# Optimization experiments

Measured on AMD Instinct MI355X. Metric: run time of the kernel, lower is better.

Reference implementation:

```python
import jax, jax.numpy as jnp
import numpy as np

EMBEDDING_DIM = 10
CONTEXT_SIZE_1 = 1
CONTEXT_SIZE_2 = 3
VOCAB = 50000
N = 1_000_000
NUM_NUMERIC = 16


def setup_inputs() -> dict:
    key = jax.random.key(0)
    ks = jax.random.split(key, 9)
    text_1 = jax.random.randint(ks[0], (N,), 0, VOCAB)
    text_2 = jax.random.randint(ks[1], (N,), 0, VOCAB)
    numeric_features = jax.random.normal(ks[2], (N, NUM_NUMERIC), dtype=jnp.float32)
    emb_table_1 = jax.random.normal(ks[3], (VOCAB, EMBEDDING_DIM), dtype=jnp.float32)
    emb_table_2 = jax.random.normal(ks[4], (VOCAB, EMBEDDING_DIM), dtype=jnp.float32)
    d_in = 2 * EMBEDDING_DIM + NUM_NUMERIC
    W1 = jax.random.normal(ks[5], (d_in, 128), dtype=jnp.float32) / np.sqrt(d_in)
    b1 = jnp.zeros((128,), dtype=jnp.float32)
    W2 = jax.random.normal(ks[6], (128, 1), dtype=jnp.float32) / np.sqrt(128.0)
    b2 = jnp.zeros((1,), dtype=jnp.float32)
    return {
        "text_1": text_1,
        "text_2": text_2,
        "numeric_features": numeric_features,
        "emb_table_1": emb_table_1,
        "emb_table_2": emb_table_2,
        "W1": W1,
        "b1": b1,
        "W2": W2,
        "b2": b2,
    }


def _contextual_embedding(ids, table, context_size):
    # mean of embeddings over window [i-cs, i+cs], clipped at sequence edges
    n = ids.shape[0]
    emb = table[ids]  # [N, D] gather
    # prefix sums with leading zero row: S[j] = sum(emb[0:j])
    S = jnp.concatenate([jnp.zeros((1, emb.shape[1]), emb.dtype),
                         jnp.cumsum(emb, axis=0)], axis=0)
    pos = jnp.arange(n)
    lo = jnp.maximum(pos - context_size, 0)
    hi = jnp.minimum(pos + context_size + 1, n)
    wsum = S[hi] - S[lo]                       # [N, D]
    count = (hi - lo).astype(emb.dtype)[:, None]
    return wsum / count


def reference(text_1, text_2, numeric_features, emb_table_1, emb_table_2, W1, b1, W2, b2):
    embed_1 = _contextual_embedding(text_1, emb_table_1, CONTEXT_SIZE_1)  # [N, 10]
    embed_2 = _contextual_embedding(text_2, emb_table_2, CONTEXT_SIZE_2)  # [N, 10]
    combined = jnp.concatenate([embed_1, embed_2, numeric_features], axis=1)
    h = jax.nn.relu(combined @ W1 + b1)
    out = h @ W2 + b2
    return jax.nn.sigmoid(out)  # [N, 1]
```

## Files before the change

kernel.cpp:

```cpp
#include <hip/hip_runtime.h>
#include <hip/hip_bf16.h>

#define EMB 10
#define DIN 36
#define HID 128
#define BM  128
#define GRID 1024

typedef __attribute__((ext_vector_type(8))) short short8;
typedef __attribute__((ext_vector_type(4))) float f32x4;

union U8 { unsigned u[4]; short8 v; };

__device__ __forceinline__ short bf16_hi(float v) {
  __hip_bfloat16 h = __float2bfloat16(v);
  return *reinterpret_cast<short*>(&h);
}
__device__ __forceinline__ float bf16_to_f(short s) {
  __hip_bfloat16 h = *reinterpret_cast<__hip_bfloat16*>(&s);
  return __bfloat162float(h);
}

__device__ __forceinline__ void split_pair(float a, float b, unsigned &hi, unsigned &lo) {
  unsigned ua = __float_as_uint(a), ub = __float_as_uint(b);
  hi = __builtin_amdgcn_perm(ub, ua, 0x07060302u);
  float ra = a - __uint_as_float(ua & 0xFFFF0000u);
  float rb = b - __uint_as_float(ub & 0xFFFF0000u);
  lo = __builtin_amdgcn_perm(__float_as_uint(rb), __float_as_uint(ra), 0x07060302u);
}

__global__ void prep_kernel(const float* __restrict__ W1, const float* __restrict__ b1,
                            short* __restrict__ Bpack) {
  int b = blockIdx.x;
  int term = b >> 4;
  int ct   = (b >> 1) & 7;
  int ks   = b & 1;
  int l = threadIdx.x;
  int col = ct * 16 + (l & 15);
  int kb  = ks * 32 + (l >> 4) * 8;
  short8 o;
#pragma unroll
  for (int e = 0; e < 8; ++e) {
    int k = kb + e;
    float v = 0.0f;
    if (k < DIN)       v = W1[k * HID + col];
    else if (k == DIN) v = b1[col];
    short hb = bf16_hi(v);
    o[e] = (term == 0) ? hb : bf16_hi(v - bf16_to_f(hb));
  }
  *(short8*)(Bpack + (size_t)(((term * 8 + ct) * 2 + ks) * 64 + l) * 8) = o;
}

__global__ __launch_bounds__(256)
void fused_kernel(const int* __restrict__ t1, const int* __restrict__ t2,
                  const float* __restrict__ numf,
                  const float* __restrict__ tab1, const float* __restrict__ tab2,
                  const short* __restrict__ Bpack,
                  const float* __restrict__ W2, const float* __restrict__ b2,
                  float* __restrict__ out, int N, int ntiles) {
  __shared__ float E1[134][11];
  __shared__ float E2[136][11];
  __shared__ float Cs[BM][22];
  __shared__ short Bs[16384];

  const int tid = threadIdx.x;
  const int wid = tid >> 6, l = tid & 63;
  const int arow = l & 15, kg = l >> 4;
  const int h2 = tid - 122;

  {
    const float4* src = (const float4*)Bpack;
    float4* dst = (float4*)Bs;
#pragma unroll
    for (int i = 0; i < 8; ++i) dst[tid + 256 * i] = src[tid + 256 * i];
  }
  float w2r[8];
#pragma unroll
  for (int ct = 0; ct < 8; ++ct) w2r[ct] = W2[ct * 16 + (l & 15)];
  const float b2v = b2[0];

  const int q = ntiles / GRID, r = ntiles % GRID;
  int tbeg, tend;
  if ((int)blockIdx.x < r) { tbeg = blockIdx.x * (q + 1); tend = tbeg + q + 1; }
  else { tbeg = r * (q + 1) + ((int)blockIdx.x - r) * q; tend = tbeg + q; }

  for (int t = tbeg; t < tend; ++t) {
    const long base = (long)t * BM;

    const long rg0 = base + (long)(wid * 2) * 16 + arow;
    const long rg1 = rg0 + 16;
    float4 qa0 = {0,0,0,0}, qa1 = {0,0,0,0}, qb0 = {0,0,0,0}, qb1 = {0,0,0,0};
    if (kg == 0) {
      if (rg0 < (long)N) qa0 = *(const float4*)(numf + rg0 * 16 + 12);
      if (rg1 < (long)N) qa1 = *(const float4*)(numf + rg1 * 16 + 12);
    } else if (kg == 2) {
      if (rg0 < (long)N) qa0 = *(const float4*)(numf + rg0 * 16);
      if (rg1 < (long)N) qa1 = *(const float4*)(numf + rg1 * 16);
    } else if (kg == 3) {
      if (rg0 < (long)N) { qa0 = *(const float4*)(numf + rg0 * 16 + 4);
                           qb0 = *(const float4*)(numf + rg0 * 16 + 8); }
      if (rg1 < (long)N) { qa1 = *(const float4*)(numf + rg1 * 16 + 4);
                           qb1 = *(const float4*)(numf + rg1 * 16 + 8); }
    }

    if (tid < 130) {
      long g = base - 1 + tid;
      if (g >= 0 && g < (long)N) {
        const float2* src = (const float2*)(tab1 + (long)t1[g] * EMB);
#pragma unroll
        for (int i = 0; i < 5; ++i) {
          float2 v = src[i];
          E1[tid][2 * i] = v.x; E1[tid][2 * i + 1] = v.y;
        }
      } else {
#pragma unroll
        for (int i = 0; i < EMB; ++i) E1[tid][i] = 0.0f;
      }
    }
    if (h2 >= 0) {
      long g = base - 3 + h2;
      if (g >= 0 && g < (long)N) {
        const float2* src = (const float2*)(tab2 + (long)t2[g] * EMB);
#pragma unroll
        for (int i = 0; i < 5; ++i) {
          float2 v = src[i];
          E2[h2][2 * i] = v.x; E2[h2][2 * i + 1] = v.y;
        }
      } else {
#pragma unroll
        for (int i = 0; i < EMB; ++i) E2[h2][i] = 0.0f;
      }
    }
    __syncthreads();

    const bool edgeblk = (base == 0) || (base + BM + 3 > (long)N);
    if (tid < 120) {
      int grp = tid / 10, d = tid - grp * 10;
      int r0 = grp * 11;
      float e[13];
#pragma unroll
      for (int i = 0; i < 13; ++i) e[i] = E1[r0 + i][d];
      if (!edgeblk) {
#pragma unroll
        for (int i = 0; i < 11; ++i) {
          int rr = r0 + i;
          if (rr < BM) Cs[rr][d] = (e[i] + e[i + 1] + e[i + 2]) * (1.0f / 3.0f);
        }
      } else {
#pragma unroll
        for (int i = 0; i < 11; ++i) {
          int rr = r0 + i;
          if (rr < BM) {
            long row = base + rr;
            long lo = row - 1; if (lo < 0) lo = 0;
            long hi = row + 2; if (hi > (long)N) hi = (long)N;
            long c = hi - lo;  if (c < 1) c = 1;
            Cs[rr][d] = (e[i] + e[i + 1] + e[i + 2]) / (float)c;
          }
        }
      }
    } else if (tid < 250) {
      int u = tid - 120;
      int grp = u / 10, d = u - grp * 10;
      int r0 = grp * 10;
      float e[16];
#pragma unroll
      for (int i = 0; i < 16; ++i) e[i] = E2[r0 + i][d];
      float w = e[0] + e[1] + e[2] + e[3] + e[4] + e[5] + e[6];
      if (!edgeblk) {
#pragma unroll
        for (int i = 0; i < 10; ++i) {
          int rr = r0 + i;
          if (rr < BM) Cs[rr][10 + d] = w * (1.0f / 7.0f);
          if (i < 9) w += e[i + 7] - e[i];
        }
      } else {
#pragma unroll
        for (int i = 0; i < 10; ++i) {
          int rr = r0 + i;
          if (rr < BM) {
            long row = base + rr;
            long lo = row - 3; if (lo < 0) lo = 0;
            long hi = row + 4; if (hi > (long)N) hi = (long)N;
            long c = hi - lo;  if (c < 1) c = 1;
            Cs[rr][10 + d] = w / (float)c;
          }
          if (i < 9) w += e[i + 7] - e[i];
        }
      }
    }
    __syncthreads();

    short8 aHi[2][2], aLo[2][2];
#pragma unroll
    for (int rtl = 0; rtl < 2; ++rtl) {
      const int rr = (wid * 2 + rtl) * 16 + arow;
      const float* crow = &Cs[rr][0];
      const float4 qa = rtl ? qa1 : qa0;
      const float4 qb = rtl ? qb1 : qb0;
      U8 h0, l0, h1, l1;
      if (kg <= 1) {
#pragma unroll
        for (int i = 0; i < 4; ++i) {
          float2 tt = *(const float2*)(crow + kg * 8 + 2 * i);
          split_pair(tt.x, tt.y, h0.u[i], l0.u[i]);
        }
      } else if (kg == 2) {
        float2 t0 = *(const float2*)(crow + 16);
        float2 t1v = *(const float2*)(crow + 18);
        split_pair(t0.x, t0.y, h0.u[0], l0.u[0]);
        split_pair(t1v.x, t1v.y, h0.u[1], l0.u[1]);
        split_pair(qa.x, qa.y, h0.u[2], l0.u[2]);
        split_pair(qa.z, qa.w, h0.u[3], l0.u[3]);
      } else {
        split_pair(qa.x, qa.y, h0.u[0], l0.u[0]);
        split_pair(qa.z, qa.w, h0.u[1], l0.u[1]);
        split_pair(qb.x, qb.y, h0.u[2], l0.u[2]);
        split_pair(qb.z, qb.w, h0.u[3], l0.u[3]);
      }
      if (kg == 0) {
        split_pair(qa.x, qa.y, h1.u[0], l1.u[0]);
        split_pair(qa.z, qa.w, h1.u[1], l1.u[1]);
        h1.u[2] = 0x00003F80u; l1.u[2] = 0u;
        h1.u[3] = 0u;          l1.u[3] = 0u;
      } else {
        h1.u[0] = h1.u[1] = h1.u[2] = h1.u[3] = 0u;
        l1.u[0] = l1.u[1] = l1.u[2] = l1.u[3] = 0u;
      }
      aHi[rtl][0] = h0.v; aLo[rtl][0] = l0.v;
      aHi[rtl][1] = h1.v; aLo[rtl][1] = l1.v;
    }

    float part[2][4] = {{0,0,0,0},{0,0,0,0}};
#pragma unroll
    for (int ct = 0; ct < 8; ++ct) {
      short8 bh0 = *(const short8*)&Bs[(size_t)(((0*8 + ct)*2 + 0)*64 + l) * 8];
      short8 bh1 = *(const short8*)&Bs[(size_t)(((0*8 + ct)*2 + 1)*64 + l) * 8];
      short8 bl0 = *(const short8*)&Bs[(size_t)(((1*8 + ct)*2 + 0)*64 + l) * 8];
      short8 bl1 = *(const short8*)&Bs[(size_t)(((1*8 + ct)*2 + 1)*64 + l) * 8];
      float w2c = w2r[ct];
#pragma unroll
      for (int rtl = 0; rtl < 2; ++rtl) {
        f32x4 acc = {0.0f, 0.0f, 0.0f, 0.0f};
        acc = __builtin_amdgcn_mfma_f32_16x16x32_bf16(aHi[rtl][0], bh0, acc, 0, 0, 0);
        acc = __builtin_amdgcn_mfma_f32_16x16x32_bf16(aLo[rtl][0], bh0, acc, 0, 0, 0);
        acc = __builtin_amdgcn_mfma_f32_16x16x32_bf16(aHi[rtl][0], bl0, acc, 0, 0, 0);
        acc = __builtin_amdgcn_mfma_f32_16x16x32_bf16(aHi[rtl][1], bh1, acc, 0, 0, 0);
        acc = __builtin_amdgcn_mfma_f32_16x16x32_bf16(aLo[rtl][1], bh1, acc, 0, 0, 0);
        acc = __builtin_amdgcn_mfma_f32_16x16x32_bf16(aHi[rtl][1], bl1, acc, 0, 0, 0);
#pragma unroll
        for (int rg = 0; rg < 4; ++rg) {
          float hv = fmaxf(acc[rg], 0.0f);
          part[rtl][rg] += hv * w2c;
        }
      }
    }
#pragma unroll
    for (int off = 1; off < 16; off <<= 1) {
#pragma unroll
      for (int rtl = 0; rtl < 2; ++rtl)
#pragma unroll
        for (int rg = 0; rg < 4; ++rg)
          part[rtl][rg] += __shfl_xor(part[rtl][rg], off, 64);
    }
    if ((l & 15) < 4) {
#pragma unroll
      for (int rtl = 0; rtl < 2; ++rtl) {
        int rt = wid * 2 + rtl;
        long grow = base + rt * 16 + (l >> 4) * 4 + (l & 15);
        if (grow < (long)N) {
          float x = part[rtl][l & 15] + b2v;
          out[grow] = 1.0f / (1.0f + exp2f(x * -1.44269504f));
        }
      }
    }
  }
}

extern "C" void kernel_launch(void* const* d_in, const int* in_sizes, int n_in,
                              void* d_out, int out_size, void* d_ws, size_t ws_size,
                              hipStream_t stream) {
  const int*   t1   = (const int*)d_in[0];
  const int*   t2   = (const int*)d_in[1];
  const float* numf = (const float*)d_in[2];
  const float* tab1 = (const float*)d_in[3];
  const float* tab2 = (const float*)d_in[4];
  const float* W1   = (const float*)d_in[5];
  const float* b1   = (const float*)d_in[6];
  const float* W2   = (const float*)d_in[7];
  const float* b2   = (const float*)d_in[8];
  float* out = (float*)d_out;
  const int N = in_sizes[0];
  short* Bpack = (short*)d_ws;

  hipLaunchKernelGGL(prep_kernel, dim3(32), dim3(64), 0, stream, W1, b1, Bpack);
  int ntiles = (N + BM - 1) / BM;
  hipLaunchKernelGGL(fused_kernel, dim3(GRID), dim3(256), 0, stream,
                     t1, t2, numf, tab1, tab2, Bpack, W2, b2, out, N, ntiles);
}
```

Baseline: 208.8 us.

## Pad embedding tables to 64B rows and launch one block per tile

Adds a repack kernel that copies both embedding tables into 16-float padded rows in workspace, so each gather reads aligned float4 vectors instead of five float2 loads. The persistent grid-stride loop over tiles is replaced by one block per 128-row tile. The shared-memory copy of the packed W1 is dropped and the B fragments are read straight from global memory. The repack adds a full pass over both tables on every call, and the padded path only runs if the workspace is large enough.

Measured after the change: 247.3 us. +18.4%, slower.

```diff
diff --git a/kernel.cpp b/kernel.cpp
--- a/kernel.cpp
+++ b/kernel.cpp
@@ -5,7 +5,7 @@
 #define DIN 36
 #define HID 128
 #define BM  128
-#define GRID 1024
+#define VOCAB_MAX 50000
 
 typedef __attribute__((ext_vector_type(8))) short short8;
 typedef __attribute__((ext_vector_type(4))) float f32x4;
@@ -51,227 +51,249 @@
   *(short8*)(Bpack + (size_t)(((term * 8 + ct) * 2 + ks) * 64 + l) * 8) = o;
 }
 
+__global__ void repack_kernel(const float* __restrict__ tab1, const float* __restrict__ tab2,
+                              float* __restrict__ tp1, float* __restrict__ tp2, int vocab) {
+  int r = blockIdx.x * 256 + threadIdx.x;
+  if (r >= vocab) return;
+  const float2* s1 = (const float2*)(tab1 + (long)r * EMB);
+  const float2* s2 = (const float2*)(tab2 + (long)r * EMB);
+  float* d1 = tp1 + (long)r * 16;
+  float* d2 = tp2 + (long)r * 16;
+#pragma unroll
+  for (int i = 0; i < 5; ++i) { *(float2*)(d1 + 2 * i) = s1[i]; }
+#pragma unroll
+  for (int i = 0; i < 5; ++i) { *(float2*)(d2 + 2 * i) = s2[i]; }
+}
+
 __global__ __launch_bounds__(256)
 void fused_kernel(const int* __restrict__ t1, const int* __restrict__ t2,
                   const float* __restrict__ numf,
                   const float* __restrict__ tab1, const float* __restrict__ tab2,
+                  const float* __restrict__ tp1, const float* __restrict__ tp2,
+                  int use_padded,
                   const short* __restrict__ Bpack,
                   const float* __restrict__ W2, const float* __restrict__ b2,
-                  float* __restrict__ out, int N, int ntiles) {
-  __shared__ float E1[134][11];
-  __shared__ float E2[136][11];
+                  float* __restrict__ out, int N) {
+  __shared__ float E1[134][12];
+  __shared__ float E2[136][12];
   __shared__ float Cs[BM][22];
-  __shared__ short Bs[16384];
 
   const int tid = threadIdx.x;
+  const long base = (long)blockIdx.x * BM;
   const int wid = tid >> 6, l = tid & 63;
   const int arow = l & 15, kg = l >> 4;
-  const int h2 = tid - 122;
-
-  {
-    const float4* src = (const float4*)Bpack;
-    float4* dst = (float4*)Bs;
-#pragma unroll
-    for (int i = 0; i < 8; ++i) dst[tid + 256 * i] = src[tid + 256 * i];
+
+  const long rg0 = base + (long)(wid * 2) * 16 + arow;
+  const long rg1 = rg0 + 16;
+  float4 qa0 = {0,0,0,0}, qa1 = {0,0,0,0}, qb0 = {0,0,0,0}, qb1 = {0,0,0,0};
+  if (kg == 0) {
+    if (rg0 < (long)N) qa0 = *(const float4*)(numf + rg0 * 16 + 12);
+    if (rg1 < (long)N) qa1 = *(const float4*)(numf + rg1 * 16 + 12);
+  } else if (kg == 2) {
+    if (rg0 < (long)N) qa0 = *(const float4*)(numf + rg0 * 16);
+    if (rg1 < (long)N) qa1 = *(const float4*)(numf + rg1 * 16);
+  } else if (kg == 3) {
+    if (rg0 < (long)N) { qa0 = *(const float4*)(numf + rg0 * 16 + 4);
+                         qb0 = *(const float4*)(numf + rg0 * 16 + 8); }
+    if (rg1 < (long)N) { qa1 = *(const float4*)(numf + rg1 * 16 + 4);
+                         qb1 = *(const float4*)(numf + rg1 * 16 + 8); }
   }
   float w2r[8];
 #pragma unroll
   for (int ct = 0; ct < 8; ++ct) w2r[ct] = W2[ct * 16 + (l & 15)];
   const float b2v = b2[0];
 
-  const int q = ntiles / GRID, r = ntiles % GRID;
-  int tbeg, tend;
-  if ((int)blockIdx.x < r) { tbeg = blockIdx.x * (q + 1); tend = tbeg + q + 1; }
-  else { tbeg = r * (q + 1) + ((int)blockIdx.x - r) * q; tend = tbeg + q; }
-
-  for (int t = tbeg; t < tend; ++t) {
-    const long base = (long)t * BM;
-
-    const long rg0 = base + (long)(wid * 2) * 16 + arow;
-    const long rg1 = rg0 + 16;
-    float4 qa0 = {0,0,0,0}, qa1 = {0,0,0,0}, qb0 = {0,0,0,0}, qb1 = {0,0,0,0};
-    if (kg == 0) {
-      if (rg0 < (long)N) qa0 = *(const float4*)(numf + rg0 * 16 + 12);
-      if (rg1 < (long)N) qa1 = *(const float4*)(numf + rg1 * 16 + 12);
-    } else if (kg == 2) {
-      if (rg0 < (long)N) qa0 = *(const float4*)(numf + rg0 * 16);
-      if (rg1 < (long)N) qa1 = *(const float4*)(numf + rg1 * 16);
-    } else if (kg == 3) {
-      if (rg0 < (long)N) { qa0 = *(const float4*)(numf + rg0 * 16 + 4);
-                           qb0 = *(const float4*)(numf + rg0 * 16 + 8); }
-      if (rg1 < (long)N) { qa1 = *(const float4*)(numf + rg1 * 16 + 4);
-                           qb1 = *(const float4*)(numf + rg1 * 16 + 8); }
-    }
-
-    if (tid < 130) {
-      long g = base - 1 + tid;
-      if (g >= 0 && g < (long)N) {
-        const float2* src = (const float2*)(tab1 + (long)t1[g] * EMB);
+  if (tid < 130) {
+    long g = base - 1 + tid;
+    if (g >= 0 && g < (long)N) {
+      long idx = t1[g];
+      if (use_padded) {
+        const float4* src = (const float4*)(tp1 + idx * 16);
+        float4 q0 = src[0], q1 = src[1];
+        float2 q2 = ((const float2*)src)[4];
+        *(float4*)&E1[tid][0] = q0;
+        *(float4*)&E1[tid][4] = q1;
+        *(float2*)&E1[tid][8] = q2;
+      } else {
+        const float2* src = (const float2*)(tab1 + idx * EMB);
 #pragma unroll
         for (int i = 0; i < 5; ++i) {
           float2 v = src[i];
           E1[tid][2 * i] = v.x; E1[tid][2 * i + 1] = v.y;
         }
-      } else {
-#pragma unroll
-        for (int i = 0; i < EMB; ++i) E1[tid][i] = 0.0f;
-      }
-    }
+      }
+    } else {
+#pragma unroll
+      for (int i = 0; i < EMB; ++i) E1[tid][i] = 0.0f;
+    }
+  }
+  {
+    int h2 = tid - 122;
     if (h2 >= 0) {
       long g = base - 3 + h2;
       if (g >= 0 && g < (long)N) {
-        const float2* src = (const float2*)(tab2 + (long)t2[g] * EMB);
-#pragma unroll
-        for (int i = 0; i < 5; ++i) {
-          float2 v = src[i];
-          E2[h2][2 * i] = v.x; E2[h2][2 * i + 1] = v.y;
+        long idx = t2[g];
+        if (use_padded) {
+          const float4* src = (const float4*)(tp2 + idx * 16);
+          float4 q0 = src[0], q1 = src[1];
+          float2 q2 = ((const float2*)src)[4];
+          *(float4*)&E2[h2][0] = q0;
+          *(float4*)&E2[h2][4] = q1;
+          *(float2*)&E2[h2][8] = q2;
+        } else {
+          const float2* src = (const float2*)(tab2 + idx * EMB);
+#pragma unroll
+          for (int i = 0; i < 5; ++i) {
+            float2 v = src[i];
+            E2[h2][2 * i] = v.x; E2[h2][2 * i + 1] = v.y;
+          }
         }
       } else {
 #pragma unroll
         for (int i = 0; i < EMB; ++i) E2[h2][i] = 0.0f;
       }
     }
-    __syncthreads();
-
-    const bool edgeblk = (base == 0) || (base + BM + 3 > (long)N);
-    if (tid < 120) {
-      int grp = tid / 10, d = tid - grp * 10;
-      int r0 = grp * 11;
-      float e[13];
-#pragma unroll
-      for (int i = 0; i < 13; ++i) e[i] = E1[r0 + i][d];
-      if (!edgeblk) {
-#pragma unroll
-        for (int i = 0; i < 11; ++i) {
-          int rr = r0 + i;
-          if (rr < BM) Cs[rr][d] = (e[i] + e[i + 1] + e[i + 2]) * (1.0f / 3.0f);
+  }
+  __syncthreads();
+
+  const bool edgeblk = (base == 0) || (base + BM + 3 > (long)N);
+  if (tid < 120) {
+    int grp = tid / 10, d = tid - grp * 10;
+    int r0 = grp * 11;
+    float e[13];
+#pragma unroll
+    for (int i = 0; i < 13; ++i) e[i] = E1[r0 + i][d];
+    if (!edgeblk) {
+#pragma unroll
+      for (int i = 0; i < 11; ++i) {
+        int rr = r0 + i;
+        if (rr < BM) Cs[rr][d] = (e[i] + e[i + 1] + e[i + 2]) * (1.0f / 3.0f);
+      }
+    } else {
+#pragma unroll
+      for (int i = 0; i < 11; ++i) {
+        int rr = r0 + i;
+        if (rr < BM) {
+          long row = base + rr;
+          long lo = row - 1; if (lo < 0) lo = 0;
+          long hi = row + 2; if (hi > (long)N) hi = (long)N;
+          long c = hi - lo;  if (c < 1) c = 1;
+          Cs[rr][d] = (e[i] + e[i + 1] + e[i + 2]) / (float)c;
         }
-      } else {
-#pragma unroll
-        for (int i = 0; i < 11; ++i) {
-          int rr = r0 + i;
-          if (rr < BM) {
-            long row = base + rr;
-            long lo = row - 1; if (lo < 0) lo = 0;
-            long hi = row + 2; if (hi > (long)N) hi = (long)N;
-            long c = hi - lo;  if (c < 1) c = 1;
-            Cs[rr][d] = (e[i] + e[i + 1] + e[i + 2]) / (float)c;
-          }
+      }
+    }
+  } else if (tid < 250) {
+    int u = tid - 120;
+    int grp = u / 10, d = u - grp * 10;
+    int r0 = grp * 10;
+    float e[16];
+#pragma unroll
+    for (int i = 0; i < 16; ++i) e[i] = E2[r0 + i][d];
+    float w = e[0] + e[1] + e[2] + e[3] + e[4] + e[5] + e[6];
+    if (!edgeblk) {
+#pragma unroll
+      for (int i = 0; i < 10; ++i) {
+        int rr = r0 + i;
+        if (rr < BM) Cs[rr][10 + d] = w * (1.0f / 7.0f);
+        if (i < 9) w += e[i + 7] - e[i];
+      }
+    } else {
+#pragma unroll
+      for (int i = 0; i < 10; ++i) {
+        int rr = r0 + i;
+        if (rr < BM) {
+          long row = base + rr;
+          long lo = row - 3; if (lo < 0) lo = 0;
+          long hi = row + 4; if (hi > (long)N) hi = (long)N;
+          long c = hi - lo;  if (c < 1) c = 1;
+          Cs[rr][10 + d] = w / (float)c;
         }
-      }
-    } else if (tid < 250) {
-      int u = tid - 120;
-      int grp = u / 10, d = u - grp * 10;
-      int r0 = grp * 10;
-      float e[16];
-#pragma unroll
-      for (int i = 0; i < 16; ++i) e[i] = E2[r0 + i][d];
-      float w = e[0] + e[1] + e[2] + e[3] + e[4] + e[5] + e[6];
-      if (!edgeblk) {
-#pragma unroll
-        for (int i = 0; i < 10; ++i) {
-          int rr = r0 + i;
-          if (rr < BM) Cs[rr][10 + d] = w * (1.0f / 7.0f);
-          if (i < 9) w += e[i + 7] - e[i];
-        }
-      } else {
-#pragma unroll
-        for (int i = 0; i < 10; ++i) {
-          int rr = r0 + i;
-          if (rr < BM) {
-            long row = base + rr;
-            long lo = row - 3; if (lo < 0) lo = 0;
-            long hi = row + 4; if (hi > (long)N) hi = (long)N;
-            long c = hi - lo;  if (c < 1) c = 1;
-            Cs[rr][10 + d] = w / (float)c;
-          }
-          if (i < 9) w += e[i + 7] - e[i];
-        }
-      }
-    }
-    __syncthreads();
-
-    short8 aHi[2][2], aLo[2][2];
+        if (i < 9) w += e[i + 7] - e[i];
+      }
+    }
+  }
+  __syncthreads();
+
+  short8 aHi[2][2], aLo[2][2];
+#pragma unroll
+  for (int rtl = 0; rtl < 2; ++rtl) {
+    const int rr = (wid * 2 + rtl) * 16 + arow;
+    const float* crow = &Cs[rr][0];
+    const float4 qa = rtl ? qa1 : qa0;
+    const float4 qb = rtl ? qb1 : qb0;
+    U8 h0, l0, h1, l1;
+    if (kg <= 1) {
+#pragma unroll
+      for (int i = 0; i < 4; ++i) {
+        float2 tt = *(const float2*)(crow + kg * 8 + 2 * i);
+        split_pair(tt.x, tt.y, h0.u[i], l0.u[i]);
+      }
+    } else if (kg == 2) {
+      float2 t0 = *(const float2*)(crow + 16);
+      float2 t1v = *(const float2*)(crow + 18);
+      split_pair(t0.x, t0.y, h0.u[0], l0.u[0]);
+      split_pair(t1v.x, t1v.y, h0.u[1], l0.u[1]);
+      split_pair(qa.x, qa.y, h0.u[2], l0.u[2]);
+      split_pair(qa.z, qa.w, h0.u[3], l0.u[3]);
+    } else {
+      split_pair(qa.x, qa.y, h0.u[0], l0.u[0]);
+      split_pair(qa.z, qa.w, h0.u[1], l0.u[1]);
+      split_pair(qb.x, qb.y, h0.u[2], l0.u[2]);
+      split_pair(qb.z, qb.w, h0.u[3], l0.u[3]);
+    }
+    if (kg == 0) {
+      split_pair(qa.x, qa.y, h1.u[0], l1.u[0]);
+      split_pair(qa.z, qa.w, h1.u[1], l1.u[1]);
+      h1.u[2] = 0x00003F80u; l1.u[2] = 0u;
+      h1.u[3] = 0u;          l1.u[3] = 0u;
+    } else {
+      h1.u[0] = h1.u[1] = h1.u[2] = h1.u[3] = 0u;
+      l1.u[0] = l1.u[1] = l1.u[2] = l1.u[3] = 0u;
+    }
+    aHi[rtl][0] = h0.v; aLo[rtl][0] = l0.v;
+    aHi[rtl][1] = h1.v; aLo[rtl][1] = l1.v;
+  }
+
+  float part[2][4] = {{0,0,0,0},{0,0,0,0}};
+#pragma unroll
+  for (int ct = 0; ct < 8; ++ct) {
+    short8 bh0 = *(const short8*)(Bpack + (size_t)(((0*8 + ct)*2 + 0)*64 + l)*8);
+    short8 bh1 = *(const short8*)(Bpack + (size_t)(((0*8 + ct)*2 + 1)*64 + l)*8);
+    short8 bl0 = *(const short8*)(Bpack + (size_t)(((1*8 + ct)*2 + 0)*64 + l)*8);
+    short8 bl1 = *(const short8*)(Bpack + (size_t)(((1*8 + ct)*2 + 1)*64 + l)*8);
+    float w2c = w2r[ct];
 #pragma unroll
     for (int rtl = 0; rtl < 2; ++rtl) {
-      const int rr = (wid * 2 + rtl) * 16 + arow;
-      const float* crow = &Cs[rr][0];
-      const float4 qa = rtl ? qa1 : qa0;
-      const float4 qb = rtl ? qb1 : qb0;
-      U8 h0, l0, h1, l1;
-      if (kg <= 1) {
-#pragma unroll
-        for (int i = 0; i < 4; ++i) {
-          float2 tt = *(const float2*)(crow + kg * 8 + 2 * i);
-          split_pair(tt.x, tt.y, h0.u[i], l0.u[i]);
-        }
-      } else if (kg == 2) {
-        float2 t0 = *(const float2*)(crow + 16);
-        float2 t1v = *(const float2*)(crow + 18);
-        split_pair(t0.x, t0.y, h0.u[0], l0.u[0]);
-        split_pair(t1v.x, t1v.y, h0.u[1], l0.u[1]);
-        split_pair(qa.x, qa.y, h0.u[2], l0.u[2]);
-        split_pair(qa.z, qa.w, h0.u[3], l0.u[3]);
-      } else {
-        split_pair(qa.x, qa.y, h0.u[0], l0.u[0]);
-        split_pair(qa.z, qa.w, h0.u[1], l0.u[1]);
-        split_pair(qb.x, qb.y, h0.u[2], l0.u[2]);
-        split_pair(qb.z, qb.w, h0.u[3], l0.u[3]);
-      }
-      if (kg == 0) {
-        split_pair(qa.x, qa.y, h1.u[0], l1.u[0]);
-        split_pair(qa.z, qa.w, h1.u[1], l1.u[1]);
-        h1.u[2] = 0x00003F80u; l1.u[2] = 0u;
-        h1.u[3] = 0u;          l1.u[3] = 0u;
-      } else {
-        h1.u[0] = h1.u[1] = h1.u[2] = h1.u[3] = 0u;
-        l1.u[0] = l1.u[1] = l1.u[2] = l1.u[3] = 0u;
-      }
-      aHi[rtl][0] = h0.v; aLo[rtl][0] = l0.v;
-      aHi[rtl][1] = h1.v; aLo[rtl][1] = l1.v;
-    }
-
-    float part[2][4] = {{0,0,0,0},{0,0,0,0}};
-#pragma unroll
-    for (int ct = 0; ct < 8; ++ct) {
-      short8 bh0 = *(const short8*)&Bs[(size_t)(((0*8 + ct)*2 + 0)*64 + l) * 8];
-      short8 bh1 = *(const short8*)&Bs[(size_t)(((0*8 + ct)*2 + 1)*64 + l) * 8];
-      short8 bl0 = *(const short8*)&Bs[(size_t)(((1*8 + ct)*2 + 0)*64 + l) * 8];
-      short8 bl1 = *(const short8*)&Bs[(size_t)(((1*8 + ct)*2 + 1)*64 + l) * 8];
-      float w2c = w2r[ct];
-#pragma unroll
-      for (int rtl = 0; rtl < 2; ++rtl) {
-        f32x4 acc = {0.0f, 0.0f, 0.0f, 0.0f};
-        acc = __builtin_amdgcn_mfma_f32_16x16x32_bf16(aHi[rtl][0], bh0, acc, 0, 0, 0);
-        acc = __builtin_amdgcn_mfma_f32_16x16x32_bf16(aLo[rtl][0], bh0, acc, 0, 0, 0);
-        acc = __builtin_amdgcn_mfma_f32_16x16x32_bf16(aHi[rtl][0], bl0, acc, 0, 0, 0);
-        acc = __builtin_amdgcn_mfma_f32_16x16x32_bf16(aHi[rtl][1], bh1, acc, 0, 0, 0);
-        acc = __builtin_amdgcn_mfma_f32_16x16x32_bf16(aLo[rtl][1], bh1, acc, 0, 0, 0);
-        acc = __builtin_amdgcn_mfma_f32_16x16x32_bf16(aHi[rtl][1], bl1, acc, 0, 0, 0);
-#pragma unroll
-        for (int rg = 0; rg < 4; ++rg) {
-          float hv = fmaxf(acc[rg], 0.0f);
-          part[rtl][rg] += hv * w2c;
-        }
-      }
-    }
-#pragma unroll
-    for (int off = 1; off < 16; off <<= 1) {
-#pragma unroll
-      for (int rtl = 0; rtl < 2; ++rtl)
-#pragma unroll
-        for (int rg = 0; rg < 4; ++rg)
-          part[rtl][rg] += __shfl_xor(part[rtl][rg], off, 64);
-    }
-    if ((l & 15) < 4) {
-#pragma unroll
-      for (int rtl = 0; rtl < 2; ++rtl) {
-        int rt = wid * 2 + rtl;
-        long grow = base + rt * 16 + (l >> 4) * 4 + (l & 15);
-        if (grow < (long)N) {
-          float x = part[rtl][l & 15] + b2v;
-          out[grow] = 1.0f / (1.0f + exp2f(x * -1.44269504f));
-        }
+      f32x4 acc = {0.0f, 0.0f, 0.0f, 0.0f};
+      acc = __builtin_amdgcn_mfma_f32_16x16x32_bf16(aHi[rtl][0], bh0, acc, 0, 0, 0);
+      acc = __builtin_amdgcn_mfma_f32_16x16x32_bf16(aLo[rtl][0], bh0, acc, 0, 0, 0);
+      acc = __builtin_amdgcn_mfma_f32_16x16x32_bf16(aHi[rtl][0], bl0, acc, 0, 0, 0);
+      acc = __builtin_amdgcn_mfma_f32_16x16x32_bf16(aHi[rtl][1], bh1, acc, 0, 0, 0);
+      acc = __builtin_amdgcn_mfma_f32_16x16x32_bf16(aLo[rtl][1], bh1, acc, 0, 0, 0);
+      acc = __builtin_amdgcn_mfma_f32_16x16x32_bf16(aHi[rtl][1], bl1, acc, 0, 0, 0);
+#pragma unroll
+      for (int rg = 0; rg < 4; ++rg) {
+        float hv = fmaxf(acc[rg], 0.0f);
+        part[rtl][rg] += hv * w2c;
+      }
+    }
+  }
+#pragma unroll
+  for (int off = 1; off < 16; off <<= 1) {
+#pragma unroll
+    for (int rtl = 0; rtl < 2; ++rtl)
+#pragma unroll
+      for (int rg = 0; rg < 4; ++rg)
+        part[rtl][rg] += __shfl_xor(part[rtl][rg], off, 64);
+  }
+  if ((l & 15) < 4) {
+#pragma unroll
+    for (int rtl = 0; rtl < 2; ++rtl) {
+      int rt = wid * 2 + rtl;
+      long grow = base + rt * 16 + (l >> 4) * 4 + (l & 15);
+      if (grow < (long)N) {
+        float x = part[rtl][l & 15] + b2v;
+        out[grow] = 1.0f / (1.0f + exp2f(x * -1.44269504f));
       }
     }
   }
@@ -291,10 +313,22 @@
   const float* b2   = (const float*)d_in[8];
   float* out = (float*)d_out;
   const int N = in_sizes[0];
+  const int vocab = in_sizes[3] / EMB;
+
   short* Bpack = (short*)d_ws;
+  const size_t padbytes = (size_t)vocab * 16 * sizeof(float);
+  const size_t need = 32768 + 2 * padbytes;
+  const int use_padded = (ws_size >= need) ? 1 : 0;
+  float* tp1 = (float*)((char*)d_ws + 32768);
+  float* tp2 = (float*)((char*)d_ws + 32768 + padbytes);
 
   hipLaunchKernelGGL(prep_kernel, dim3(32), dim3(64), 0, stream, W1, b1, Bpack);
-  int ntiles = (N + BM - 1) / BM;
-  hipLaunchKernelGGL(fused_kernel, dim3(GRID), dim3(256), 0, stream,
-                     t1, t2, numf, tab1, tab2, Bpack, W2, b2, out, N, ntiles);
-}
+  if (use_padded) {
+    hipLaunchKernelGGL(repack_kernel, dim3((vocab + 255) / 256), dim3(256), 0, stream,
+                       tab1, tab2, tp1, tp2, vocab);
+  }
+  int nblk = (N + BM - 1) / BM;
+  hipLaunchKernelGGL(fused_kernel, dim3(nblk), dim3(256), 0, stream,
+                     t1, t2, numf, tab1, tab2, tp1, tp2, use_padded,
+                     Bpack, W2, b2, out, N);
+}
```
